# Optimization experiments

Hardware: AMD Instinct MI355X
Metric: run time of the kernel (lower is better)

Reference implementation:

```python
import jax, jax.numpy as jnp
import numpy as np

B, M, D = 16, 100000, 128
OUT = 128  # out_features; in_features = 2*D


def setup_inputs() -> dict:
    key = jax.random.key(0)
    k1, k2, k3, k4 = jax.random.split(key, 4)
    s1 = 1.0 / np.sqrt(2 * D)  # ~ torch Linear default init scale
    s2 = 1.0 / np.sqrt(OUT)
    return {
        "xx_anchor": jax.random.normal(k1, (B, D), dtype=jnp.float32),
        "input": jax.random.normal(k2, (M, D), dtype=jnp.float32),
        "adj": jnp.zeros((1, 1), dtype=jnp.float32),  # densified then unused in forward math
        "W1": jax.random.normal(k3, (OUT, 2 * D), dtype=jnp.float32) * s1,
        "W2": jax.random.normal(k4, (1, OUT), dtype=jnp.float32) * s2,
    }


def reference(xx_anchor, input, adj, W1, W2):
    d = input.shape[1]
    # concat(q_vec, input) @ W1.T  ==  q @ W1[:, :d].T  +  input @ W1[:, d:].T
    # (avoids materializing the [B, m, 2d] concat tensor; same math)
    anchor_part = xx_anchor @ W1[:, :d].T          # [B, out]
    node_part = input @ W1[:, d:].T                # [m, out]
    h = jax.nn.relu(anchor_part[:, None, :] + node_part[None, :, :])  # [B, m, out]
    scores = jnp.einsum('bmo,o->bm', h, W2[0])     # linear2 -> [B, m]
    atten = jax.nn.softmax(scores, axis=1)          # softmax over node dim
    v_vec = jnp.einsum('bm,md->bd', atten, input)   # weighted sum pooling
    return v_vec
```

## Files before the change

### kernel.cpp

```cpp
#include <hip/hip_runtime.h>
#include <hip/hip_bf16.h>
#include <math.h>


typedef __attribute__((ext_vector_type(8))) short bf16x8;
typedef __attribute__((ext_vector_type(4))) float f32x4;

__device__ __forceinline__ short f2bs(float f) {
    __hip_bfloat16 h = __float2bfloat16(f);
    return *reinterpret_cast<short*>(&h);
}
__device__ __forceinline__ float bs2f(ushort u) {
    union { unsigned int i; float f; } v; v.i = ((unsigned)u) << 16; return v.f;
}
__device__ __forceinline__ bf16x8 pack8(float4 a, float4 b) {
    bf16x8 r;
    r[0] = f2bs(a.x); r[1] = f2bs(a.y); r[2] = f2bs(a.z); r[3] = f2bs(a.w);
    r[4] = f2bs(b.x); r[5] = f2bs(b.y); r[6] = f2bs(b.z); r[7] = f2bs(b.w);
    return r;
}

__global__ __launch_bounds__(256) void kA(const float* __restrict__ W1,
                                          const float* __restrict__ xx,
                                          ushort* __restrict__ w1b,
                                          float* __restrict__ A) {
    const int bi = blockIdx.x, t = threadIdx.x;
    if (bi < 64) {
        int idx = bi * 256 + t;
        int o = idx >> 7, d = idx & 127;
        w1b[idx] = (ushort)f2bs(W1[o * 256 + 128 + d]);
        return;
    }
    __shared__ float xxs[16 * 132];
    __shared__ float w1s[16 * 132];
    const int og0 = (bi - 64) * 16;
#pragma unroll
    for (int i = 0; i < 2; ++i) {
        int idx = t + 256 * i;
        int r = idx >> 5, c4 = (idx & 31) << 2;
        *(float4*)&xxs[r * 132 + c4] = *(const float4*)&xx[r * 128 + c4];
        *(float4*)&w1s[r * 132 + c4] = *(const float4*)&W1[(og0 + r) * 256 + c4];
    }
    __syncthreads();
    const int ol = t >> 4, b = t & 15;
    float acc = 0.f;
#pragma unroll
    for (int d4 = 0; d4 < 32; ++d4) {
        float4 xv = *(float4*)&xxs[b * 132 + d4 * 4];
        float4 wv = *(float4*)&w1s[ol * 132 + d4 * 4];
        acc += xv.x * wv.x + xv.y * wv.y + xv.z * wv.z + xv.w * wv.w;
    }
    A[b * 128 + og0 + ol] = acc;
}

__global__ __launch_bounds__(256, 3) void kB(
    const float* __restrict__ in, const ushort* __restrict__ w1b,
    const float* __restrict__ W2, const float* __restrict__ A,
    float* __restrict__ lsum_g, ushort* __restrict__ pacc, int M) {
    __shared__ ushort ins[128 * 136];
    __shared__ float As[16 * 128];
    __shared__ ushort pb[16 * 136];

    const int tid = threadIdx.x, bid = blockIdx.x;
    const int m0 = bid * 128;
    const int w = tid >> 6, lane = tid & 63;
    const int c = lane & 15, q = lane >> 4;
    const int lim = (M - m0 < 128) ? (M - m0) : 128;

    const int r0 = w * 32 + c;
    const int r1 = r0 + 16;
    const bool v0 = r0 < lim, v1 = r1 < lim;
    int cr0 = m0 + r0; if (cr0 > M - 1) cr0 = M - 1;
    int cr1 = m0 + r1; if (cr1 > M - 1) cr1 = M - 1;
    const float* __restrict__ row0 = in + (size_t)cr0 * 128;
    const float* __restrict__ row1 = in + (size_t)cr1 * 128;

    const int kq = q * 8;
    float4 pA0 = *(const float4*)&row0[kq];       float4 pA1 = *(const float4*)&row0[kq + 4];
    float4 pB0 = *(const float4*)&row0[kq + 32];  float4 pB1 = *(const float4*)&row0[kq + 36];
    float4 pC0 = *(const float4*)&row0[kq + 64];  float4 pC1 = *(const float4*)&row0[kq + 68];
    float4 pD0 = *(const float4*)&row0[kq + 96];  float4 pD1 = *(const float4*)&row0[kq + 100];
    float4 qA0 = *(const float4*)&row1[kq];       float4 qA1 = *(const float4*)&row1[kq + 4];
    float4 qB0 = *(const float4*)&row1[kq + 32];  float4 qB1 = *(const float4*)&row1[kq + 36];
    float4 qC0 = *(const float4*)&row1[kq + 64];  float4 qC1 = *(const float4*)&row1[kq + 68];
    float4 qD0 = *(const float4*)&row1[kq + 96];  float4 qD1 = *(const float4*)&row1[kq + 100];

#pragma unroll
    for (int i = 0; i < 2; ++i) {
        int idx = tid + 256 * i;
        *(float4*)&As[idx * 4] = *(const float4*)&A[idx * 4];
    }

    f32x4 acc[2][8];
#pragma unroll
    for (int mt = 0; mt < 2; ++mt)
#pragma unroll
        for (int ot = 0; ot < 8; ++ot) acc[mt][ot] = (f32x4){0.f, 0.f, 0.f, 0.f};

#define NP_STEP(kb, Pa, Pb, Qa, Qb)                                               \
    {                                                                             \
        const int k0 = (kb) * 32 + kq;                                            \
        bf16x8 bv0 = pack8(Pa, Pb);                                               \
        bf16x8 bv1 = pack8(Qa, Qb);                                               \
        *(bf16x8*)&ins[r0 * 136 + k0] = bv0;                                      \
        *(bf16x8*)&ins[r1 * 136 + k0] = bv1;                                      \
        _Pragma("unroll")                                                         \
        for (int ot = 0; ot < 8; ++ot) {                                          \
            bf16x8 av = *(const bf16x8*)(w1b + (ot * 16 + c) * 128 + k0);         \
            acc[0][ot] = __builtin_amdgcn_mfma_f32_16x16x32_bf16(av, bv0, acc[0][ot], 0, 0, 0); \
            acc[1][ot] = __builtin_amdgcn_mfma_f32_16x16x32_bf16(av, bv1, acc[1][ot], 0, 0, 0); \
        }                                                                         \
    }
    NP_STEP(0, pA0, pA1, qA0, qA1)
    NP_STEP(1, pB0, pB1, qB0, qB1)
    NP_STEP(2, pC0, pC1, qC0, qC1)
    NP_STEP(3, pD0, pD1, qD0, qD1)
#undef NP_STEP

    f32x4 w2q[8];
#pragma unroll
    for (int ot = 0; ot < 8; ++ot) {
        f32x4 wv = *(const f32x4*)&W2[ot * 16 + q * 4];
        w2q[ot] = wv * 0.5f;
    }
    __syncthreads();

    float sm0 = 0.f, sm1 = 0.f;
#pragma unroll
    for (int ot = 0; ot < 8; ++ot)
#pragma unroll
        for (int r = 0; r < 4; ++r) {
            sm0 += acc[0][ot][r] * w2q[ot][r];
            sm1 += acc[1][ot][r] * w2q[ot][r];
        }

#pragma unroll
    for (int b = 0; b < 16; ++b) {
        float sa0 = sm0, sa1 = sm1, sb0 = 0.f, sb1 = 0.f;
#pragma unroll
        for (int ot = 0; ot < 8; ot += 2) {
            f32x4 aq0 = *(f32x4*)&As[b * 128 + ot * 16 + q * 4];
            f32x4 aq1 = *(f32x4*)&As[b * 128 + (ot + 1) * 16 + q * 4];
#pragma unroll
            for (int r = 0; r < 4; ++r) {
                sa0 += fabsf(acc[0][ot][r]     + aq0[r]) * w2q[ot][r];
                sa1 += fabsf(acc[1][ot][r]     + aq0[r]) * w2q[ot][r];
                sb0 += fabsf(acc[0][ot + 1][r] + aq1[r]) * w2q[ot + 1][r];
                sb1 += fabsf(acc[1][ot + 1][r] + aq1[r]) * w2q[ot + 1][r];
            }
        }
        float s0 = sa0 + sb0, s1 = sa1 + sb1;
        s0 += __shfl_xor(s0, 16, 64);
        s0 += __shfl_xor(s0, 32, 64);
        s1 += __shfl_xor(s1, 16, 64);
        s1 += __shfl_xor(s1, 32, 64);
        if (q == (b & 3)) {
            pb[b * 136 + r0] = (ushort)f2bs(v0 ? __expf(s0) : 0.f);
            pb[b * 136 + r1] = (ushort)f2bs(v1 ? __expf(s1) : 0.f);
        }
    }
    __syncthreads();

    f32x4 pd[2];
    pd[0] = (f32x4){0.f, 0.f, 0.f, 0.f};
    pd[1] = (f32x4){0.f, 0.f, 0.f, 0.f};
#pragma unroll
    for (int ks = 0; ks < 4; ++ks) {
        bf16x8 pf = *(const bf16x8*)&pb[c * 136 + ks * 32 + q * 8];
#pragma unroll
        for (int t = 0; t < 2; ++t) {
            const int dloc = w * 32 + t * 16 + c;
            bf16x8 bf;
#pragma unroll
            for (int j = 0; j < 8; ++j)
                bf[j] = (short)ins[(ks * 32 + q * 8 + j) * 136 + dloc];
            pd[t] = __builtin_amdgcn_mfma_f32_16x16x32_bf16(pf, bf, pd[t], 0, 0, 0);
        }
    }
#pragma unroll
    for (int t = 0; t < 2; ++t)
#pragma unroll
        for (int r = 0; r < 4; ++r)
            pacc[((size_t)bid * 16 + q * 4 + r) * 128 + w * 32 + t * 16 + c] =
                (ushort)f2bs(pd[t][r]);

    {
        const int bb = tid >> 4, jj = tid & 15;
        const ushort* pr = &pb[bb * 136 + jj * 8];
        float part = 0.f;
#pragma unroll
        for (int j2 = 0; j2 < 8; ++j2) part += bs2f(pr[j2]);
#pragma unroll
        for (int off = 1; off < 16; off <<= 1) part += __shfl_xor(part, off, 64);
        if (jj == 0) lsum_g[bid * 16 + bb] = part;
    }
}

__global__ __launch_bounds__(256) void kC1(
    const float* __restrict__ lsum_g, const ushort* __restrict__ pacc,
    float* __restrict__ pacc2, float* __restrict__ lsum2, int nb) {
    const int b = blockIdx.x >> 4, s = blockIdx.x & 15;
    const int t = threadIdx.x;
    __shared__ float reda[2 * 128];
    __shared__ float redl[2];
    const int cs = (nb + 15) >> 4;
    const int blk0 = s * cs;
    int blk1 = blk0 + cs; if (blk1 > nb) blk1 = nb;
    const int dd = t & 127, h = t >> 7;
    float ac = 0.f, ls = 0.f;
    for (int blk = blk0 + h; blk < blk1; blk += 2) {
        ac += bs2f(pacc[((size_t)blk * 16 + b) * 128 + dd]);
        ls += lsum_g[blk * 16 + b];
    }
    reda[h * 128 + dd] = ac;
    if (dd == 0) redl[h] = ls;
    __syncthreads();
    if (h == 0) {
        pacc2[((size_t)s * 16 + b) * 128 + dd] = reda[dd] + reda[128 + dd];
        if (dd == 0) lsum2[s * 16 + b] = redl[0] + redl[1];
    }
}

__global__ void kFin(const float* __restrict__ pacc2, const float* __restrict__ lsum2,
                     float* __restrict__ out) {
    const int b = blockIdx.x, t = threadIdx.x;
    float ac = 0.f, ls = 0.f;
#pragma unroll
    for (int s = 0; s < 16; ++s) {
        ac += pacc2[((size_t)s * 16 + b) * 128 + t];
        ls += lsum2[s * 16 + b];
    }
    out[b * 128 + t] = ac / ls;
}

extern "C" void kernel_launch(void* const* d_in, const int* in_sizes, int n_in,
                              void* d_out, int out_size, void* d_ws, size_t ws_size,
                              hipStream_t stream) {
    const float* xx = (const float*)d_in[0];
    const float* in = (const float*)d_in[1];
    const float* W1 = (const float*)d_in[3];
    const float* W2 = (const float*)d_in[4];
    float* out = (float*)d_out;

    const int M = in_sizes[1] / 128;
    const int nb = (M + 127) / 128;

    float* ws = (float*)d_ws;
    float* A      = ws;
    float* lsum_g = A + 2048;
    float* pacc2  = lsum_g + (size_t)nb * 16;
    float* lsum2  = pacc2 + 256 * 128;
    ushort* w1b   = (ushort*)(lsum2 + 256);
    ushort* pacc  = w1b + 16384;

    kA  <<<72, 256, 0, stream>>>(W1, xx, w1b, A);
    kB  <<<nb, 256, 0, stream>>>(in, w1b, W2, A, lsum_g, pacc, M);
    kC1 <<<256, 256, 0, stream>>>(lsum_g, pacc, pacc2, lsum2, nb);
    kFin<<<16, 128, 0, stream>>>(pacc2, lsum2, out);
}
```

Measured before the change: 136.6 us.

## Read anchor part directly from global in kB and merge final reductions

New measurement: 139.0 us. About the same (+1.8%).

```diff
diff --git a/kernel.cpp b/kernel.cpp
--- a/kernel.cpp
+++ b/kernel.cpp
@@ -58,7 +58,6 @@
     const float* __restrict__ W2, const float* __restrict__ A,
     float* __restrict__ lsum_g, ushort* __restrict__ pacc, int M) {
     __shared__ ushort ins[128 * 136];
-    __shared__ float As[16 * 128];
     __shared__ ushort pb[16 * 136];
 
     const int tid = threadIdx.x, bid = blockIdx.x;
@@ -84,12 +83,6 @@
     float4 qB0 = *(const float4*)&row1[kq + 32];  float4 qB1 = *(const float4*)&row1[kq + 36];
     float4 qC0 = *(const float4*)&row1[kq + 64];  float4 qC1 = *(const float4*)&row1[kq + 68];
     float4 qD0 = *(const float4*)&row1[kq + 96];  float4 qD1 = *(const float4*)&row1[kq + 100];
-
-#pragma unroll
-    for (int i = 0; i < 2; ++i) {
-        int idx = tid + 256 * i;
-        *(float4*)&As[idx * 4] = *(const float4*)&A[idx * 4];
-    }
 
     f32x4 acc[2][8];
 #pragma unroll
@@ -123,7 +116,6 @@
         f32x4 wv = *(const f32x4*)&W2[ot * 16 + q * 4];
         w2q[ot] = wv * 0.5f;
     }
-    __syncthreads();
 
     float sm0 = 0.f, sm1 = 0.f;
 #pragma unroll
@@ -134,13 +126,14 @@
             sm1 += acc[1][ot][r] * w2q[ot][r];
         }
 
-#pragma unroll
+#pragma unroll 4
     for (int b = 0; b < 16; ++b) {
+        const float* __restrict__ Ab = A + b * 128 + q * 4;
         float sa0 = sm0, sa1 = sm1, sb0 = 0.f, sb1 = 0.f;
 #pragma unroll
         for (int ot = 0; ot < 8; ot += 2) {
-            f32x4 aq0 = *(f32x4*)&As[b * 128 + ot * 16 + q * 4];
-            f32x4 aq1 = *(f32x4*)&As[b * 128 + (ot + 1) * 16 + q * 4];
+            f32x4 aq0 = *(const f32x4*)&Ab[ot * 16];
+            f32x4 aq1 = *(const f32x4*)&Ab[(ot + 1) * 16];
 #pragma unroll
             for (int r = 0; r < 4; ++r) {
                 sa0 += fabsf(acc[0][ot][r]     + aq0[r]) * w2q[ot][r];
@@ -196,41 +189,38 @@
     }
 }
 
-__global__ __launch_bounds__(256) void kC1(
+__global__ __launch_bounds__(256) void kD(
     const float* __restrict__ lsum_g, const ushort* __restrict__ pacc,
-    float* __restrict__ pacc2, float* __restrict__ lsum2, int nb) {
-    const int b = blockIdx.x >> 4, s = blockIdx.x & 15;
+    float* __restrict__ out, int nb) {
+    const int b = blockIdx.x >> 4, ds = blockIdx.x & 15;
     const int t = threadIdx.x;
-    __shared__ float reda[2 * 128];
-    __shared__ float redl[2];
-    const int cs = (nb + 15) >> 4;
-    const int blk0 = s * cs;
-    int blk1 = blk0 + cs; if (blk1 > nb) blk1 = nb;
-    const int dd = t & 127, h = t >> 7;
-    float ac = 0.f, ls = 0.f;
-    for (int blk = blk0 + h; blk < blk1; blk += 2) {
-        ac += bs2f(pacc[((size_t)blk * 16 + b) * 128 + dd]);
-        ls += lsum_g[blk * 16 + b];
-    }
-    reda[h * 128 + dd] = ac;
-    if (dd == 0) redl[h] = ls;
-    __syncthreads();
-    if (h == 0) {
-        pacc2[((size_t)s * 16 + b) * 128 + dd] = reda[dd] + reda[128 + dd];
-        if (dd == 0) lsum2[s * 16 + b] = redl[0] + redl[1];
-    }
-}
-
-__global__ void kFin(const float* __restrict__ pacc2, const float* __restrict__ lsum2,
-                     float* __restrict__ out) {
-    const int b = blockIdx.x, t = threadIdx.x;
-    float ac = 0.f, ls = 0.f;
-#pragma unroll
-    for (int s = 0; s < 16; ++s) {
-        ac += pacc2[((size_t)s * 16 + b) * 128 + t];
-        ls += lsum2[s * 16 + b];
-    }
-    out[b * 128 + t] = ac / ls;
+    const int dj = t & 7, g = t >> 3;
+    const int d = ds * 8 + dj;
+    float ac = 0.f;
+    for (int blk = g; blk < nb; blk += 32)
+        ac += bs2f(pacc[((size_t)blk * 16 + b) * 128 + d]);
+    float ls = 0.f;
+    for (int blk = t; blk < nb; blk += 256) ls += lsum_g[(size_t)blk * 16 + b];
+
+    __shared__ float reda[256];
+    __shared__ float redl[256];
+    reda[t] = ac; redl[t] = ls;
+    __syncthreads();
+    if (t < 128) { reda[t] += reda[t + 128]; redl[t] += redl[t + 128]; }
+    __syncthreads();
+    if (t < 64) { reda[t] += reda[t + 64]; redl[t] += redl[t + 64]; }
+    __syncthreads();
+    if (t < 32) { reda[t] += reda[t + 32]; redl[t] += redl[t + 32]; }
+    __syncthreads();
+    if (t < 16) { reda[t] += reda[t + 16]; redl[t] += redl[t + 16]; }
+    __syncthreads();
+    if (t < 8) {
+        float a = reda[t] + reda[t + 8];
+        float l = 0.f;
+#pragma unroll
+        for (int i = 0; i < 16; ++i) l += redl[i];
+        out[b * 128 + ds * 8 + t] = a / l;
+    }
 }
 
 extern "C" void kernel_launch(void* const* d_in, const int* in_sizes, int n_in,
@@ -248,13 +238,10 @@
     float* ws = (float*)d_ws;
     float* A      = ws;
     float* lsum_g = A + 2048;
-    float* pacc2  = lsum_g + (size_t)nb * 16;
-    float* lsum2  = pacc2 + 256 * 128;
-    ushort* w1b   = (ushort*)(lsum2 + 256);
+    ushort* w1b   = (ushort*)(lsum_g + (size_t)nb * 16);
     ushort* pacc  = w1b + 16384;
 
-    kA  <<<72, 256, 0, stream>>>(W1, xx, w1b, A);
-    kB  <<<nb, 256, 0, stream>>>(in, w1b, W2, A, lsum_g, pacc, M);
-    kC1 <<<256, 256, 0, stream>>>(lsum_g, pacc, pacc2, lsum2, nb);
-    kFin<<<16, 128, 0, stream>>>(pacc2, lsum2, out);
-}
+    kA <<<72, 256, 0, stream>>>(W1, xx, w1b, A);
+    kB <<<nb, 256, 0, stream>>>(in, w1b, W2, A, lsum_g, pacc, M);
+    kD <<<256, 256, 0, stream>>>(lsum_g, pacc, out, nb);
+}
```
